# Kernel tuning notes

Measured on AMD Instinct MI355X. Metric: run time of the kernel, lower is better.

Reference implementation:

```python
import jax, jax.numpy as jnp
import numpy as np

F8 = jnp.float8_e4m3fn
FP8_MAX = 448.0  # max representable magnitude of e4m3fn


def setup_inputs() -> dict:
    key = jax.random.key(0)
    kx, kw, kb = jax.random.split(key, 3)
    x = jax.random.normal(kx, (4, 4096, 2048), dtype=jnp.float32)
    w = jax.random.normal(kw, (8192, 2048), dtype=jnp.float32) * 0.02
    bias = (jax.random.normal(kb, (8192,), dtype=jnp.float32) * 0.01).astype(jnp.float16)
    return {"x": x, "w": w, "bias": bias}


def _quantize_per_tensor(t):
    """Dynamic per-tensor symmetric fp8 quantization (mirrors the torch code).
    Returns (t_fp8, inv_scale) with inv_scale = amax / 448."""
    amax = jnp.max(jnp.abs(t))
    scale = (FP8_MAX / jnp.maximum(amax, 1e-12)).astype(jnp.float32)
    scale = jax.lax.stop_gradient(scale)  # torch computes scales under no_grad
    t_fp8 = (t * scale).astype(F8)
    return t_fp8, (1.0 / scale)


def reference(x, w, bias):
    in_features = w.shape[1]
    out_features = w.shape[0]
    x2d = x.reshape(-1, in_features)            # [M, K]
    x_fp8, inv_sx = _quantize_per_tensor(x2d)   # activation: dynamic per-tensor
    w_fp8, inv_sw = _quantize_per_tensor(w)     # weight: pre-quantized buffer + scale_w
    # _scaled_mm: fp8 GEMM accumulated in fp32, output scaled by scale_a*scale_b, cast to fp16
    acc = jnp.matmul(x_fp8.astype(jnp.float32), w_fp8.astype(jnp.float32).T)  # [M, N]
    out = (acc * (inv_sx * inv_sw)).astype(jnp.float16)
    out = out + bias  # fp16 bias epilogue
    return out.reshape(*x.shape[:-1], out_features)
```

## Files before the change

### kernel.cpp

```cpp
#include <hip/hip_runtime.h>
#include <hip/hip_fp16.h>
#include <stdint.h>
#include <stddef.h>

typedef float f32x4 __attribute__((ext_vector_type(4)));
typedef int   i32x8 __attribute__((ext_vector_type(8)));

#define GLOBAL_AS __attribute__((address_space(1)))
#define LDS_AS    __attribute__((address_space(3)))

__device__ __forceinline__ void gload_lds16(const void* g, void* l) {
    __builtin_amdgcn_global_load_lds((const GLOBAL_AS void*)g,
                                     (LDS_AS void*)l, 16, 0, 0);
}

__global__ void amax2_kernel(const float* __restrict__ x, size_t nx4,
                             const float* __restrict__ w, size_t nw4,
                             float* __restrict__ scal, int xblocks, int wblocks) {
    int b = blockIdx.x;
    const float4* p4; size_t n4; float* out; int nb; int bb;
    if (b < xblocks) { p4 = (const float4*)x; n4 = nx4; out = scal;     nb = xblocks; bb = b; }
    else             { p4 = (const float4*)w; n4 = nw4; out = scal + 1; nb = wblocks; bb = b - xblocks; }
    float m = 0.f;
    for (size_t i = (size_t)bb * blockDim.x + threadIdx.x; i < n4;
         i += (size_t)nb * blockDim.x) {
        float4 v = p4[i];
        m = fmaxf(m, fmaxf(fmaxf(fabsf(v.x), fabsf(v.y)),
                           fmaxf(fabsf(v.z), fabsf(v.w))));
    }
    #pragma unroll
    for (int off = 32; off > 0; off >>= 1)
        m = fmaxf(m, __shfl_down(m, off, 64));
    __shared__ float sm[4];
    int wid = threadIdx.x >> 6;
    if ((threadIdx.x & 63) == 0) sm[wid] = m;
    __syncthreads();
    if (threadIdx.x == 0) {
        m = fmaxf(fmaxf(sm[0], sm[1]), fmaxf(sm[2], sm[3]));
        atomicMax((unsigned int*)out, __float_as_uint(m));
    }
}

__global__ void quant2_kernel(const float* __restrict__ x, const float* __restrict__ w,
                              const float* __restrict__ scal,
                              uint32_t* __restrict__ qx, uint32_t* __restrict__ qw,
                              int xblocks) {
    int b = blockIdx.x;
    const float* src; uint32_t* dst; float sc; size_t i;
    if (b < xblocks) { src = x; dst = qx; sc = 448.f / fmaxf(scal[0], 1e-12f);
                       i = (size_t)b * blockDim.x + threadIdx.x; }
    else             { src = w; dst = qw; sc = 448.f / fmaxf(scal[1], 1e-12f);
                       i = (size_t)(b - xblocks) * blockDim.x + threadIdx.x; }
    const float4* s4 = (const float4*)src + i * 4;
    uint32_t r[4];
    #pragma unroll
    for (int j = 0; j < 4; ++j) {
        float4 v = s4[j];
        uint32_t u = __builtin_amdgcn_cvt_pk_fp8_f32(v.x * sc, v.y * sc, 0u, false);
        u = __builtin_amdgcn_cvt_pk_fp8_f32(v.z * sc, v.w * sc, u, true);
        r[j] = u;
    }
    uint4 out; out.x = r[0]; out.y = r[1]; out.z = r[2]; out.w = r[3];
    *(uint4*)(dst + i * 4) = out;
}

#define BM 128
#define BN 128
#define BKB 128

__global__ __launch_bounds__(256) void gemm_mxfp8_kernel(
    const uint8_t* __restrict__ Aq,
    const uint8_t* __restrict__ Bq,
    const float* __restrict__ scal,
    const float* __restrict__ bias,
    float* __restrict__ C,
    int M, int N, int K)
{
    __shared__ __align__(16) uint8_t As[BM * BKB];
    __shared__ __align__(16) uint8_t Bs[BN * BKB];

    const int tid  = threadIdx.x;
    const int wid  = tid >> 6;
    const int lane = tid & 63;
    const int wm = wid >> 1, wn = wid & 1;
    const int bn = blockIdx.x, bm = blockIdx.y;
    const int r16 = lane & 15, hi = lane >> 4;

    const int srow  = wid * 8 + (lane >> 3);
    const int schunk = ((lane & 7) ^ (lane >> 3)) << 4;
    const uint8_t* Abase = Aq + (size_t)(bm * BM + srow) * K + schunk;
    const uint8_t* Bbase = Bq + (size_t)(bn * BN + srow) * K + schunk;

    const int swz = r16 & 7;
    const int u0 = ((hi * 2)     ^ swz) << 4;
    const int u1 = ((hi * 2 + 1) ^ swz) << 4;

    f32x4 acc[4][4] = {};

    for (int k0 = 0; k0 < K; k0 += BKB) {
        #pragma unroll
        for (int rho = 0; rho < 4; ++rho) {
            gload_lds16(Abase + (size_t)rho * 32 * K + k0,
                        As + rho * 4096 + wid * 1024);
            gload_lds16(Bbase + (size_t)rho * 32 * K + k0,
                        Bs + rho * 4096 + wid * 1024);
        }
        __syncthreads();

        i32x8 a[4], b[4];
        #pragma unroll
        for (int mi = 0; mi < 4; ++mi) {
            const uint8_t* pa = As + (wm * 64 + mi * 16 + r16) * BKB;
            int4 qa0 = *(const int4*)(pa + u0);
            int4 qa1 = *(const int4*)(pa + u1);
            a[mi] = (i32x8){qa0.x, qa0.y, qa0.z, qa0.w,
                            qa1.x, qa1.y, qa1.z, qa1.w};
            const uint8_t* pb = Bs + (wn * 64 + mi * 16 + r16) * BKB;
            int4 qb0 = *(const int4*)(pb + u0);
            int4 qb1 = *(const int4*)(pb + u1);
            b[mi] = (i32x8){qb0.x, qb0.y, qb0.z, qb0.w,
                            qb1.x, qb1.y, qb1.z, qb1.w};
        }

        #pragma unroll
        for (int mi = 0; mi < 4; ++mi)
            #pragma unroll
            for (int nj = 0; nj < 4; ++nj)
                acc[mi][nj] = __builtin_amdgcn_mfma_scale_f32_16x16x128_f8f6f4(
                    a[mi], b[nj], acc[mi][nj],
                    0, 0, 0, 0x7F7F7F7F, 0, 0x7F7F7F7F);
        __syncthreads();
    }

    const float sx = 448.f / fmaxf(scal[0], 1e-12f);
    const float sw = 448.f / fmaxf(scal[1], 1e-12f);
    const float inv = (1.f / sx) * (1.f / sw);

    #pragma unroll
    for (int mi = 0; mi < 4; ++mi) {
        #pragma unroll
        for (int nj = 0; nj < 4; ++nj) {
            int col = bn * BN + wn * 64 + nj * 16 + r16;
            __half hb = __float2half(bias[col]);
            #pragma unroll
            for (int r = 0; r < 4; ++r) {
                int row = bm * BM + wm * 64 + mi * 16 + hi * 4 + r;
                float v = acc[mi][nj][r] * inv;
                __half h = __hadd(__float2half(v), hb);
                C[(size_t)row * N + col] = __half2float(h);
            }
        }
    }
}

extern "C" void kernel_launch(void* const* d_in, const int* in_sizes, int n_in,
                              void* d_out, int out_size, void* d_ws, size_t ws_size,
                              hipStream_t stream) {
    const float* x    = (const float*)d_in[0];
    const float* w    = (const float*)d_in[1];
    const float* bias = (const float*)d_in[2];
    float* out = (float*)d_out;

    const int N = in_sizes[2];
    const int K = in_sizes[1] / N;
    const int M = in_sizes[0] / K;

    uint8_t* ws = (uint8_t*)d_ws;
    float* scal = (float*)ws;
    uint8_t* Aq = ws + 256;
    uint8_t* Bq = Aq + (size_t)M * K;

    hipMemsetAsync(scal, 0, 8, stream);

    const int axb = 2048, awb = 1024;
    amax2_kernel<<<axb + awb, 256, 0, stream>>>(x, (size_t)M * K / 4,
                                                w, (size_t)N * K / 4,
                                                scal, axb, awb);

    int qxb = (int)((size_t)M * K / 16 / 256);
    int qwb = (int)((size_t)N * K / 16 / 256);
    quant2_kernel<<<qxb + qwb, 256, 0, stream>>>(x, w, scal,
                                                 (uint32_t*)Aq, (uint32_t*)Bq, qxb);

    dim3 grid(N / BN, M / BM);
    gemm_mxfp8_kernel<<<grid, 256, 0, stream>>>(Aq, Bq, scal, bias, out, M, N, K);
}
```

Before: 445.5 us.

## Double-buffer A in LDS and stream B tiles directly into registers

```diff
diff --git a/kernel.cpp b/kernel.cpp
--- a/kernel.cpp
+++ b/kernel.cpp
@@ -68,7 +68,7 @@
 #define BN 128
 #define BKB 128
 
-__global__ __launch_bounds__(256) void gemm_mxfp8_kernel(
+__global__ __launch_bounds__(256) void gemm_mxfp8_bs(
     const uint8_t* __restrict__ Aq,
     const uint8_t* __restrict__ Bq,
     const float* __restrict__ scal,
@@ -76,8 +76,7 @@
     float* __restrict__ C,
     int M, int N, int K)
 {
-    __shared__ __align__(16) uint8_t As[BM * BKB];
-    __shared__ __align__(16) uint8_t Bs[BN * BKB];
+    __shared__ __align__(16) uint8_t As[2][BM * BKB];
 
     const int tid  = threadIdx.x;
     const int wid  = tid >> 6;
@@ -89,48 +88,77 @@
     const int srow  = wid * 8 + (lane >> 3);
     const int schunk = ((lane & 7) ^ (lane >> 3)) << 4;
     const uint8_t* Abase = Aq + (size_t)(bm * BM + srow) * K + schunk;
-    const uint8_t* Bbase = Bq + (size_t)(bn * BN + srow) * K + schunk;
 
     const int swz = r16 & 7;
     const int u0 = ((hi * 2)     ^ swz) << 4;
     const int u1 = ((hi * 2 + 1) ^ swz) << 4;
 
+    const uint8_t* Brow0 = Bq + (size_t)(bn * BN + wn * 64 + r16) * K + hi * 32;
+    const uint8_t* Brow1 = Brow0 + (size_t)16 * K;
+    const uint8_t* Brow2 = Brow0 + (size_t)32 * K;
+    const uint8_t* Brow3 = Brow0 + (size_t)48 * K;
+
+#define STAGE_A(bufi, t)                                                          \
+  { _Pragma("unroll") for (int rho_ = 0; rho_ < 4; ++rho_)                        \
+      gload_lds16(Abase + (size_t)rho_ * 32 * K + (t) * BKB,                      \
+                  As[bufi] + rho_ * 4096 + wid * 1024); }
+
+#define BLOADS(B0, B1, B2, B3, koff)                                              \
+  { ((int4*)&(B0))[0] = *(const int4*)(Brow0 + (koff));                           \
+    ((int4*)&(B0))[1] = *(const int4*)(Brow0 + (koff) + 16);                      \
+    ((int4*)&(B1))[0] = *(const int4*)(Brow1 + (koff));                           \
+    ((int4*)&(B1))[1] = *(const int4*)(Brow1 + (koff) + 16);                      \
+    ((int4*)&(B2))[0] = *(const int4*)(Brow2 + (koff));                           \
+    ((int4*)&(B2))[1] = *(const int4*)(Brow2 + (koff) + 16);                      \
+    ((int4*)&(B3))[0] = *(const int4*)(Brow3 + (koff));                           \
+    ((int4*)&(B3))[1] = *(const int4*)(Brow3 + (koff) + 16); }
+
+#define LDA2(bufc, q0, q1)                                                        \
+  { const uint8_t* p0_ = As[bufc] + (wm * 64 + (q0) * 16 + r16) * BKB;            \
+    ((int4*)&a0)[0] = *(const int4*)(p0_ + u0);                                   \
+    ((int4*)&a0)[1] = *(const int4*)(p0_ + u1);                                   \
+    const uint8_t* p1_ = As[bufc] + (wm * 64 + (q1) * 16 + r16) * BKB;            \
+    ((int4*)&a1)[0] = *(const int4*)(p1_ + u0);                                   \
+    ((int4*)&a1)[1] = *(const int4*)(p1_ + u1); }
+
+#define MM1(am, bf, qq, jj)                                                       \
+  acc[qq][jj] = __builtin_amdgcn_mfma_scale_f32_16x16x128_f8f6f4(                 \
+      am, bf, acc[qq][jj], 0, 0, 0, 0x7F7F7F7F, 0, 0x7F7F7F7F);
+
+#define MFMA8(B0, B1, B2, B3, q0, q1)                                             \
+  MM1(a0, B0, q0, 0) MM1(a0, B1, q0, 1) MM1(a0, B2, q0, 2) MM1(a0, B3, q0, 3)    \
+  MM1(a1, B0, q1, 0) MM1(a1, B1, q1, 1) MM1(a1, B2, q1, 2) MM1(a1, B3, q1, 3)
+
+#define VMB(n) do { asm volatile("s_waitcnt vmcnt(" #n ")" ::: "memory");         \
+    __builtin_amdgcn_s_barrier(); } while (0)
+
     f32x4 acc[4][4] = {};
-
-    for (int k0 = 0; k0 < K; k0 += BKB) {
-        #pragma unroll
-        for (int rho = 0; rho < 4; ++rho) {
-            gload_lds16(Abase + (size_t)rho * 32 * K + k0,
-                        As + rho * 4096 + wid * 1024);
-            gload_lds16(Bbase + (size_t)rho * 32 * K + k0,
-                        Bs + rho * 4096 + wid * 1024);
-        }
-        __syncthreads();
-
-        i32x8 a[4], b[4];
-        #pragma unroll
-        for (int mi = 0; mi < 4; ++mi) {
-            const uint8_t* pa = As + (wm * 64 + mi * 16 + r16) * BKB;
-            int4 qa0 = *(const int4*)(pa + u0);
-            int4 qa1 = *(const int4*)(pa + u1);
-            a[mi] = (i32x8){qa0.x, qa0.y, qa0.z, qa0.w,
-                            qa1.x, qa1.y, qa1.z, qa1.w};
-            const uint8_t* pb = Bs + (wn * 64 + mi * 16 + r16) * BKB;
-            int4 qb0 = *(const int4*)(pb + u0);
-            int4 qb1 = *(const int4*)(pb + u1);
-            b[mi] = (i32x8){qb0.x, qb0.y, qb0.z, qb0.w,
-                            qb1.x, qb1.y, qb1.z, qb1.w};
-        }
-
-        #pragma unroll
-        for (int mi = 0; mi < 4; ++mi)
-            #pragma unroll
-            for (int nj = 0; nj < 4; ++nj)
-                acc[mi][nj] = __builtin_amdgcn_mfma_scale_f32_16x16x128_f8f6f4(
-                    a[mi], b[nj], acc[mi][nj],
-                    0, 0, 0, 0x7F7F7F7F, 0, 0x7F7F7F7F);
-        __syncthreads();
-    }
+    i32x8 a0, a1, be0, be1, be2, be3, bo0, bo1, bo2, bo3;
+
+    BLOADS(be0, be1, be2, be3, 0u);
+    STAGE_A(0, 0);
+
+    const int NT = K / BKB;
+    for (int t = 0; t < NT - 2; t += 2) {
+        BLOADS(bo0, bo1, bo2, bo3, (uint32_t)(t + 1) * BKB);
+        VMB(8);
+        STAGE_A(1, t + 1);
+        LDA2(0, 0, 1); MFMA8(be0, be1, be2, be3, 0, 1);
+        LDA2(0, 2, 3); MFMA8(be0, be1, be2, be3, 2, 3);
+        BLOADS(be0, be1, be2, be3, (uint32_t)(t + 2) * BKB);
+        VMB(8);
+        STAGE_A(0, t + 2);
+        LDA2(1, 0, 1); MFMA8(bo0, bo1, bo2, bo3, 0, 1);
+        LDA2(1, 2, 3); MFMA8(bo0, bo1, bo2, bo3, 2, 3);
+    }
+    BLOADS(bo0, bo1, bo2, bo3, (uint32_t)(NT - 1) * BKB);
+    VMB(8);
+    STAGE_A(1, NT - 1);
+    LDA2(0, 0, 1); MFMA8(be0, be1, be2, be3, 0, 1);
+    LDA2(0, 2, 3); MFMA8(be0, be1, be2, be3, 2, 3);
+    VMB(0);
+    LDA2(1, 0, 1); MFMA8(bo0, bo1, bo2, bo3, 0, 1);
+    LDA2(1, 2, 3); MFMA8(bo0, bo1, bo2, bo3, 2, 3);
 
     const float sx = 448.f / fmaxf(scal[0], 1e-12f);
     const float sw = 448.f / fmaxf(scal[1], 1e-12f);
@@ -183,5 +211,5 @@
                                                  (uint32_t*)Aq, (uint32_t*)Bq, qxb);
 
     dim3 grid(N / BN, M / BM);
-    gemm_mxfp8_kernel<<<grid, 256, 0, stream>>>(Aq, Bq, scal, bias, out, M, N, K);
-}
+    gemm_mxfp8_bs<<<grid, 256, 0, stream>>>(Aq, Bq, scal, bias, out, M, N, K);
+}
```

After: 678.0 us. 52.2% more time.
